# Kernel tuning notes

Hardware: AMD Instinct MI355X
Metric: run time of the kernel (lower is better)

The kernel has to match this reference:

```python
import jax, jax.numpy as jnp
import numpy as np

B, T, N, F_IN = 8, 16, 1000, 16
E = 16000
H, D = 4, 32          # heads, gat_hidden_shape
HL = 64               # lstm hidden
OUT = 8
NEG_SLOPE = 0.2       # PyG GATConv default


def setup_inputs() -> dict:
    key = jax.random.key(0)
    ks = jax.random.split(key, 10)
    def init(k, shape, fan):
        return (jax.random.normal(k, shape, jnp.float32) / np.sqrt(fan)).astype(jnp.float32)
    x = jax.random.normal(ks[0], (B, T, N, F_IN), jnp.float32)
    edge_index = jax.random.randint(ks[1], (2, E), 0, N)
    W_gat = init(ks[2], (F_IN, H * D), F_IN)       # GATConv lin weight
    att_src = init(ks[3], (H, D), D)
    att_dst = init(ks[4], (H, D), D)
    b_gat = jnp.zeros((H * D,), jnp.float32)
    W_ih = init(ks[5], (4 * HL, H * D), H * D)     # LSTM, gate order i,f,g,o
    W_hh = init(ks[6], (4 * HL, HL), HL)
    b_ih = jnp.zeros((4 * HL,), jnp.float32)
    b_hh = jnp.zeros((4 * HL,), jnp.float32)
    W_clf = init(ks[7], (OUT, HL), HL)
    b_clf = jnp.zeros((OUT,), jnp.float32)
    return {"x": x, "edge_index": edge_index, "W_gat": W_gat, "att_src": att_src,
            "att_dst": att_dst, "b_gat": b_gat, "W_ih": W_ih, "W_hh": W_hh,
            "b_ih": b_ih, "b_hh": b_hh, "W_clf": W_clf, "b_clf": b_clf}


def reference(x, edge_index, W_gat, att_src, att_dst, b_gat,
              W_ih, W_hh, b_ih, b_hh, W_clf, b_clf):
    Bx, Tx, Nx, Fx = x.shape
    x_flat = x.reshape(Bx * Tx, Nx, Fx)
    # PyG GATConv adds self-loops by default
    loop = jnp.arange(Nx)
    src = jnp.concatenate([edge_index[0], loop])
    dst = jnp.concatenate([edge_index[1], loop])

    def gat_graph(xg):  # xg: [N, F]
        xp = (xg @ W_gat).reshape(Nx, H, D)                 # [N,H,D]
        a_s = jnp.einsum('nhd,hd->nh', xp, att_src)         # [N,H]
        a_d = jnp.einsum('nhd,hd->nh', xp, att_dst)
        e = jax.nn.leaky_relu(a_s[src] + a_d[dst], NEG_SLOPE)  # [E+N,H]
        m = jax.ops.segment_max(e, dst, num_segments=Nx)       # per-target softmax
        ex = jnp.exp(e - m[dst])
        denom = jax.ops.segment_sum(ex, dst, num_segments=Nx)
        alpha = ex / denom[dst]                                # [E+N,H]
        out = jax.ops.segment_sum(alpha[..., None] * xp[src], dst, num_segments=Nx)
        return out.reshape(Nx, H * D) + b_gat                  # [N, H*D]

    gat = jax.vmap(gat_graph)(x_flat)          # [B*T, N, H*D]
    gat = jax.nn.relu(gat)
    pooled = gat.max(axis=1)                   # global_max_pool -> [B*T, H*D]
    seq = pooled.reshape(Bx, Tx, H * D)

    h0 = jnp.zeros((Bx, HL), jnp.float32)
    c0 = jnp.zeros((Bx, HL), jnp.float32)

    def step(carry, xt):  # xt: [B, H*D]
        h, c = carry
        gates = xt @ W_ih.T + h @ W_hh.T + b_ih + b_hh
        i, f, g, o = jnp.split(gates, 4, axis=-1)
        i, f, o = jax.nn.sigmoid(i), jax.nn.sigmoid(f), jax.nn.sigmoid(o)
        g = jnp.tanh(g)
        c = f * c + i * g
        h = o * jnp.tanh(c)
        return (h, c), None

    (hT, _), _ = jax.lax.scan(step, (h0, c0), seq.transpose(1, 0, 2))
    return hT @ W_clf.T + b_clf                # [B, OUT]
```

## Files before the change

### kernel.cpp

```cpp
#include <hip/hip_runtime.h>
#include <hip/hip_bf16.h>
#include <stdint.h>

namespace {
constexpr int kB = 8, kT = 16, kN = 1000, kF = 16;
constexpr int kE = 16000;
constexpr int kH = 4, kHD = 128;
constexpr int kHL = 64, kOUT = 8;
constexpr int kG = kB * kT;
constexpr float kNeg = 0.2f;
constexpr int kNB = 25;
constexpr int kNPB = 40;
constexpr int kPre = 1024;
constexpr int kNPW = 32;
constexpr int kBCAP = 64;

constexpr size_t CX_WG   = 0;
constexpr size_t CX_ATS  = CX_WG   + 2048;
constexpr size_t CX_ATD  = CX_ATS  + 128;
constexpr size_t CX_BG   = CX_ATD  + 128;
constexpr size_t CX_WIH  = CX_BG   + 128;
constexpr size_t CX_WHH  = CX_WIH  + 32768;
constexpr size_t CX_BIH  = CX_WHH  + 16384;
constexpr size_t CX_BHH  = CX_BIH  + 256;
constexpr size_t CX_WCLF = CX_BHH  + 256;
constexpr size_t CX_BCLF = CX_WCLF + 512;
constexpr size_t CX_TOTAL = CX_BCLF + 8;

constexpr size_t OFF_FLAG  = 0;
constexpr size_t OFF_ROW   = 256;
constexpr size_t OFF_COL   = 4352;
constexpr size_t OFF_POOL  = 68608;
constexpr size_t OFF_CANON = 134400;
constexpr size_t OFF_AS    = 239872;
constexpr size_t OFF_PPART = OFF_AS + (size_t)kG * 288000;
constexpr size_t PPART_BYTES = (size_t)kG * kNB * kHD * 4;
constexpr size_t OFF_BUCKET = OFF_PPART + PPART_BYTES;
constexpr size_t BUCKET_BYTES = (size_t)kN * kBCAP * 4;

constexpr int kSetupBlocks = 41;
}

typedef float v2f __attribute__((ext_vector_type(2)));

__device__ __forceinline__ float bf2f(unsigned short u) {
    return __uint_as_float(((uint32_t)u) << 16);
}
__device__ __forceinline__ float blo(uint32_t u) { return __uint_as_float(u << 16); }
__device__ __forceinline__ float bhi(uint32_t u) { return __uint_as_float(u & 0xffff0000u); }
__device__ __forceinline__ unsigned short f2bf(float f) {
    uint32_t u = __float_as_uint(f);
    uint32_t r = (u + 0x7fff + ((u >> 16) & 1)) >> 16;
    return (unsigned short)r;
}
__device__ __forceinline__ float sigm(float x) { return 1.f / (1.f + __expf(-x)); }

__device__ __forceinline__ int detect_isf(const unsigned short* xs, int t,
                                          int nthr, int* sh_cnt) {
    if (t == 0) *sh_cnt = 0;
    __syncthreads();
    int loc = 0;
    for (int i = t; i < 512; i += nthr) {
        unsigned short u = xs[i];
        int ex = (u >> 7) & 0xff;
        if (u == 0 || (ex >= 97 && ex <= 143)) loc++;
    }
    atomicAdd(sh_cnt, loc);
    __syncthreads();
    return (*sh_cnt >= 410) ? 0 : 1;
}

struct ConvArgs {
    const unsigned short* src[10];
    int n[10];
};

__global__ __launch_bounds__(256) void mega_setup(
        const void* __restrict__ xraw, const int* __restrict__ ei,
        ConvArgs ca,
        const unsigned short* __restrict__ WgR,
        const unsigned short* __restrict__ atsR,
        const unsigned short* __restrict__ atdR,
        int* __restrict__ flag, int* __restrict__ rowdeg, int* __restrict__ col,
        int* __restrict__ bucket, int use_bucket,
        unsigned short* __restrict__ canon,
        unsigned short* __restrict__ xp_all,
        float* __restrict__ as_all, float* __restrict__ ad_all,
        unsigned int* __restrict__ pooled) {
    const int t = threadIdx.x;
    const unsigned short* xs = (const unsigned short*)xraw;

    if (blockIdx.x < 8) {
        __shared__ int dcnt;
        const int isf = detect_isf(xs, t, 256, &dcnt);
        if (blockIdx.x == 0 && t == 0) *flag = isf;
        const int gid = (int)blockIdx.x * 256 + t;
        size_t base = 0;
        for (int s = 0; s < 10; ++s) {
            const int n = ca.n[s];
            if (isf) {
                const float* fp = (const float*)ca.src[s];
                for (int i = gid; i < n; i += 2048) canon[base + i] = f2bf(fp[i]);
            } else {
                const unsigned short* sp = ca.src[s];
                for (int i = gid; i < n; i += 2048) canon[base + i] = sp[i];
            }
            base += (size_t)n;
        }
    } else if (blockIdx.x == 8) {
        for (int i = t; i < kG * kHD; i += 256) pooled[i] = 0u;
    } else if (blockIdx.x < kSetupBlocks) {
        if (use_bucket) {
            const int gid = (int)(blockIdx.x - 9) * 256 + t;
            const int* srcp = ei;
            const int* dstp = ei + kE;
            for (int e = gid; e < kE; e += 32 * 256) {
                const int d = dstp[e];
                const int pos = atomicAdd(&rowdeg[d], 1);
                if (pos < kBCAP) bucket[d * kBCAP + pos] = srcp[e];
            }
        } else if (blockIdx.x == 9) {
            __shared__ int cnt[1024];
            __shared__ int wtot[4];
            const int lane = t & 63, w = t >> 6;
            for (int i = t; i < 1024; i += 256) cnt[i] = 0;
            __syncthreads();
            const int* dst = ei + kE;
            for (int e = t; e < kE; e += 256) atomicAdd(&cnt[dst[e]], 1);
            __syncthreads();
            const int n0 = 4 * t;
            int c0 = cnt[n0], c1 = cnt[n0 + 1], c2 = cnt[n0 + 2], c3 = cnt[n0 + 3];
            int s0 = c0, s1 = s0 + c1, s2 = s1 + c2, s3 = s2 + c3;
            int tot = s3;
#pragma unroll
            for (int sft = 1; sft < 64; sft <<= 1) {
                int v = __shfl_up(tot, sft, 64);
                if (lane >= sft) tot += v;
            }
            if (lane == 63) wtot[w] = tot;
            __syncthreads();
            int wexcl = 0;
            for (int j = 0; j < w; ++j) wexcl += wtot[j];
            const int excl = wexcl + tot - s3;
            if (t == 0) rowdeg[0] = 0;
            if (n0 < kN) {
                rowdeg[n0 + 1] = excl + s0;
                rowdeg[n0 + 2] = excl + s1;
                rowdeg[n0 + 3] = excl + s2;
                rowdeg[n0 + 4] = excl + s3;
            }
            __syncthreads();
            cnt[n0] = excl; cnt[n0 + 1] = excl + s0;
            cnt[n0 + 2] = excl + s1; cnt[n0 + 3] = excl + s2;
            __syncthreads();
            for (int e = t; e < kE; e += 256) {
                int d0 = dst[e];
                int pos = atomicAdd(&cnt[d0], 1);
                col[pos] = ei[e];
            }
        }
    } else {
        __shared__ int dcnt;
        const int isf = detect_isf(xs, t, 256, &dcnt);
        const int lane = t & 63;
        const int wv = t >> 6;
        const int wid = (int)(blockIdx.x - kSetupBlocks) * 4 + wv;

        float wA[kF], wB[kF];
        float as0, as1, ad0, ad1;
        if (isf) {
            const float* wf = (const float*)WgR;
#pragma unroll
            for (int f = 0; f < kF; ++f) {
                const float2 wp = ((const float2*)(wf + (size_t)f * kHD))[lane];
                wA[f] = wp.x; wB[f] = wp.y;
            }
            const float2 sv = ((const float2*)atsR)[lane];
            as0 = sv.x; as1 = sv.y;
            const float2 dv2 = ((const float2*)atdR)[lane];
            ad0 = dv2.x; ad1 = dv2.y;
        } else {
            const uint32_t* w32 = (const uint32_t*)WgR;
#pragma unroll
            for (int f = 0; f < kF; ++f) {
                const uint32_t u = w32[f * 64 + lane];
                wA[f] = blo(u); wB[f] = bhi(u);
            }
            const uint32_t us = ((const uint32_t*)atsR)[lane];
            as0 = blo(us); as1 = bhi(us);
            const uint32_t ud = ((const uint32_t*)atdR)[lane];
            ad0 = blo(ud); ad1 = bhi(ud);
        }

        uint32_t* xp32 = (uint32_t*)xp_all;
        const int nEnd = min(wid * kNPW + kNPW, kG * kN);
        for (int node = wid * kNPW; node < nEnd; ++node) {
            float xv[kF];
            if (isf) {
                const float4* xr4 = (const float4*)((const float*)xraw + (size_t)node * kF);
                const float4 x0 = xr4[0], x1 = xr4[1], x2 = xr4[2], x3 = xr4[3];
                xv[0] = x0.x; xv[1] = x0.y; xv[2]  = x0.z; xv[3]  = x0.w;
                xv[4] = x1.x; xv[5] = x1.y; xv[6]  = x1.z; xv[7]  = x1.w;
                xv[8] = x2.x; xv[9] = x2.y; xv[10] = x2.z; xv[11] = x2.w;
                xv[12] = x3.x; xv[13] = x3.y; xv[14] = x3.z; xv[15] = x3.w;
            } else {
                const uint4* xr4 = (const uint4*)(xs + (size_t)node * kF);
                const uint4 q0 = xr4[0], q1 = xr4[1];
                xv[0]  = blo(q0.x); xv[1]  = bhi(q0.x);
                xv[2]  = blo(q0.y); xv[3]  = bhi(q0.y);
                xv[4]  = blo(q0.z); xv[5]  = bhi(q0.z);
                xv[6]  = blo(q0.w); xv[7]  = bhi(q0.w);
                xv[8]  = blo(q1.x); xv[9]  = bhi(q1.x);
                xv[10] = blo(q1.y); xv[11] = bhi(q1.y);
                xv[12] = blo(q1.z); xv[13] = bhi(q1.z);
                xv[14] = blo(q1.w); xv[15] = bhi(q1.w);
            }
            float vA = 0.f, vB = 0.f;
#pragma unroll
            for (int f = 0; f < kF; ++f) {
                vA = fmaf(xv[f], wA[f], vA);
                vB = fmaf(xv[f], wB[f], vB);
            }
            xp32[(size_t)node * 64 + lane] =
                (uint32_t)f2bf(vA) | ((uint32_t)f2bf(vB) << 16);
            float aS = vA * as0 + vB * as1;
            float aD = vA * ad0 + vB * ad1;
#pragma unroll
            for (int sft = 1; sft < 16; sft <<= 1) {
                aS += __shfl_xor(aS, sft, 64);
                aD += __shfl_xor(aD, sft, 64);
            }
            if ((lane & 15) == 0) {
                as_all[(size_t)node * kH + (lane >> 4)] = aS;
                ad_all[(size_t)node * kH + (lane >> 4)] = aD;
            }
        }
    }
}

__global__ __launch_bounds__(256) void gat_aggregate(
        const int* __restrict__ rowdeg, const int* __restrict__ col,
        const int* __restrict__ bucket, int use_bucket,
        const unsigned short* __restrict__ xp,
        const float* __restrict__ a_s, const float* __restrict__ a_d,
        const unsigned short* __restrict__ bg,
        unsigned int* __restrict__ pooled,
        float* __restrict__ part, int use_part) {
    __shared__ float2 colal[4][4][68];
    __shared__ float pm[4][kHD];

    const int w = threadIdx.x >> 6;
    const int lane = threadIdx.x & 63;
    const int sub = lane >> 4;
    const int cl = lane & 15;
    const int hh = cl >> 2;
    const int xcd = blockIdx.x & 7;
    const int j = blockIdx.x >> 3;
    const int gl = xcd + 8 * (j / kNB);
    const int blk = j % kNB;
    const size_t gn = (size_t)gl * kN;
    const char* xpcl = (const char*)(xp + gn * kHD) + cl * 16;
    const float4* as4 = (const float4*)a_s + gn;
    const float4* ad4 = (const float4*)a_d + gn;
    const uint32_t* bg32 = (const uint32_t*)bg;
    float bgv[8];
#pragma unroll
    for (int jb = 0; jb < 4; ++jb) {
        uint32_t u = bg32[cl * 4 + jb];
        bgv[2 * jb] = blo(u);
        bgv[2 * jb + 1] = bhi(u);
    }
    float pool[8];
#pragma unroll
    for (int jb = 0; jb < 8; ++jb) pool[jb] = 0.f;

    for (int it = 0; it < 10; ++it) {
        const int n = blk * kNPB + it * 4 + w;
        int r0, deg;
        if (use_bucket) {
            r0 = n * kBCAP;
            deg = min(rowdeg[n], kBCAP);
        } else {
            r0 = rowdeg[n];
            deg = rowdeg[n + 1] - r0;
        }
        const int* colb = use_bucket ? bucket : col;
        const int E = deg + 1;
        const float4 dv = ad4[n];
        v2f acc2[4];
#pragma unroll
        for (int jb = 0; jb < 4; ++jb) acc2[jb] = (v2f){0.f, 0.f};
        float dh = 0.f;

        for (int base = 0; base < E; base += 64) {
            const int cnt = min(64, E - base);
            const int cntP = (cnt + 3) & ~3;
            if (lane < cntP) {
                const int eg = base + lane;
                const bool act = lane < cnt;
                const int s = (act && eg < deg) ? colb[r0 + eg] : n;
                float p0 = 0.f, p1 = 0.f, p2 = 0.f, p3 = 0.f;
                if (act) {
                    const float4 av = as4[s];
                    float t0 = av.x + dv.x, t1 = av.y + dv.y;
                    float t2 = av.z + dv.z, t3 = av.w + dv.w;
                    t0 = t0 > 0.f ? t0 : kNeg * t0;
                    t1 = t1 > 0.f ? t1 : kNeg * t1;
                    t2 = t2 > 0.f ? t2 : kNeg * t2;
                    t3 = t3 > 0.f ? t3 : kNeg * t3;
                    p0 = __expf(t0); p1 = __expf(t1);
                    p2 = __expf(t2); p3 = __expf(t3);
                }
                const float cf = __int_as_float(s << 8);
                colal[w][0][lane] = make_float2(cf, p0);
                colal[w][1][lane] = make_float2(cf, p1);
                colal[w][2][lane] = make_float2(cf, p2);
                colal[w][3][lane] = make_float2(cf, p3);
            }
            int e0 = 0;
            for (; e0 + 8 <= cntP; e0 += 8) {
                const float2 cA = colal[w][hh][e0 + sub];
                const float2 cB = colal[w][hh][e0 + 4 + sub];
                const uint4 uA = *(const uint4*)(xpcl + __float_as_int(cA.x));
                const uint4 uB = *(const uint4*)(xpcl + __float_as_int(cB.x));
                const float aA = cA.y, aB = cB.y;
                const v2f aA2 = {aA, aA}, aB2 = {aB, aB};
                acc2[0] += aA2 * (v2f){blo(uA.x), bhi(uA.x)};
                acc2[1] += aA2 * (v2f){blo(uA.y), bhi(uA.y)};
                acc2[2] += aA2 * (v2f){blo(uA.z), bhi(uA.z)};
                acc2[3] += aA2 * (v2f){blo(uA.w), bhi(uA.w)};
                acc2[0] += aB2 * (v2f){blo(uB.x), bhi(uB.x)};
                acc2[1] += aB2 * (v2f){blo(uB.y), bhi(uB.y)};
                acc2[2] += aB2 * (v2f){blo(uB.z), bhi(uB.z)};
                acc2[3] += aB2 * (v2f){blo(uB.w), bhi(uB.w)};
                dh += aA + aB;
            }
            if (e0 < cntP) {
                const float2 cA = colal[w][hh][e0 + sub];
                const uint4 uA = *(const uint4*)(xpcl + __float_as_int(cA.x));
                const float aA = cA.y;
                const v2f aA2 = {aA, aA};
                acc2[0] += aA2 * (v2f){blo(uA.x), bhi(uA.x)};
                acc2[1] += aA2 * (v2f){blo(uA.y), bhi(uA.y)};
                acc2[2] += aA2 * (v2f){blo(uA.z), bhi(uA.z)};
                acc2[3] += aA2 * (v2f){blo(uA.w), bhi(uA.w)};
                dh += aA;
            }
        }
        float acc[8];
#pragma unroll
        for (int jb = 0; jb < 4; ++jb) {
            acc[2 * jb] = acc2[jb].x;
            acc[2 * jb + 1] = acc2[jb].y;
        }
#pragma unroll
        for (int jb = 0; jb < 8; ++jb) {
            acc[jb] += __shfl_xor(acc[jb], 16, 64);
            acc[jb] += __shfl_xor(acc[jb], 32, 64);
        }
        dh += __shfl_xor(dh, 16, 64);
        dh += __shfl_xor(dh, 32, 64);
        const float inv = 1.f / dh;
#pragma unroll
        for (int jb = 0; jb < 8; ++jb) {
            const float o = acc[jb] * inv + bgv[jb];
            pool[jb] = fmaxf(pool[jb], o > 0.f ? o : 0.f);
        }
    }
    if (sub == 0) {
#pragma unroll
        for (int jb = 0; jb < 8; ++jb) pm[w][cl * 8 + jb] = pool[jb];
    }
    __syncthreads();
    if (w == 0 && sub == 0) {
        if (use_part) {
            float* dst = part + ((size_t)gl * kNB + blk) * kHD;
#pragma unroll
            for (int jb = 0; jb < 8; ++jb) {
                const int c = cl * 8 + jb;
                dst[c] = fmaxf(fmaxf(pm[0][c], pm[1][c]), fmaxf(pm[2][c], pm[3][c]));
            }
        } else {
            const size_t gp = (size_t)gl * kHD;
#pragma unroll
            for (int jb = 0; jb < 8; ++jb) {
                const int c = cl * 8 + jb;
                float vmax = fmaxf(fmaxf(pm[0][c], pm[1][c]), fmaxf(pm[2][c], pm[3][c]));
                atomicMax(pooled + gp + c, __float_as_uint(vmax));
            }
        }
    }
}

__global__ __launch_bounds__(256) void lstm_head(
        const float* __restrict__ pooled, const float* __restrict__ part,
        int use_part,
        const unsigned short* __restrict__ Wih,
        const unsigned short* __restrict__ Whh,
        const unsigned short* __restrict__ bih,
        const unsigned short* __restrict__ bhh,
        const unsigned short* __restrict__ Wclf,
        const unsigned short* __restrict__ bclf,
        const int* __restrict__ flag,
        void* __restrict__ out) {
    const int b = blockIdx.x;
    const int r = threadIdx.x;
    __shared__ float xt[kHD];
    __shared__ float hs[kHL];
    __shared__ float gates[4 * kHL];

    uint32_t wih[64];
    const uint32_t* pw = (const uint32_t*)(Wih + (size_t)r * kHD);
#pragma unroll
    for (int j = 0; j < 64; ++j) wih[j] = pw[j];
    uint32_t whh[32];
    const uint32_t* ph = (const uint32_t*)(Whh + (size_t)r * kHL);
#pragma unroll
    for (int j = 0; j < 32; ++j) whh[j] = ph[j];
    const float bias = bf2f(bih[r]) + bf2f(bhh[r]);

    float c_st = 0.f;
    if (r < kHL) hs[r] = 0.f;
    __syncthreads();

    for (int t = 0; t < kT; ++t) {
        const size_t g = (size_t)b * kT + t;
        if (r < kHD) {
            if (use_part) {
                const float* ps = part + g * kNB * kHD + r;
                float v = ps[0];
#pragma unroll
                for (int k = 1; k < kNB; ++k) v = fmaxf(v, ps[(size_t)k * kHD]);
                xt[r] = v;
            } else {
                xt[r] = pooled[g * kHD + r];
            }
        }
        __syncthreads();
        float a0 = 0.f, a1 = 0.f, a2 = 0.f, a3 = 0.f;
#pragma unroll
        for (int j = 0; j < 64; j += 4) {
            uint32_t u0 = wih[j], u1 = wih[j + 1], u2 = wih[j + 2], u3 = wih[j + 3];
            a0 += blo(u0) * xt[2 * j + 0] + bhi(u0) * xt[2 * j + 1];
            a1 += blo(u1) * xt[2 * j + 2] + bhi(u1) * xt[2 * j + 3];
            a2 += blo(u2) * xt[2 * j + 4] + bhi(u2) * xt[2 * j + 5];
            a3 += blo(u3) * xt[2 * j + 6] + bhi(u3) * xt[2 * j + 7];
        }
#pragma unroll
        for (int j = 0; j < 32; j += 4) {
            uint32_t u0 = whh[j], u1 = whh[j + 1], u2 = whh[j + 2], u3 = whh[j + 3];
            a0 += blo(u0) * hs[2 * j + 0] + bhi(u0) * hs[2 * j + 1];
            a1 += blo(u1) * hs[2 * j + 2] + bhi(u1) * hs[2 * j + 3];
            a2 += blo(u2) * hs[2 * j + 4] + bhi(u2) * hs[2 * j + 5];
            a3 += blo(u3) * hs[2 * j + 6] + bhi(u3) * hs[2 * j + 7];
        }
        gates[r] = bias + (a0 + a1) + (a2 + a3);
        __syncthreads();
        if (r < kHL) {
            const float iv = sigm(gates[r]);
            const float fv = sigm(gates[kHL + r]);
            const float gv = tanhf(gates[2 * kHL + r]);
            const float ov = sigm(gates[3 * kHL + r]);
            c_st = fv * c_st + iv * gv;
            hs[r] = ov * tanhf(c_st);
        }
        __syncthreads();
    }
    if (r < kOUT) {
        float acc = bf2f(bclf[r]);
#pragma unroll
        for (int k = 0; k < kHL; ++k) acc += hs[k] * bf2f(Wclf[r * kHL + k]);
        if (*flag) ((float*)out)[b * kOUT + r] = acc;
        else ((__hip_bfloat16*)out)[b * kOUT + r] = __float2bfloat16(acc);
    }
}

extern "C" void kernel_launch(void* const* d_in, const int* in_sizes, int n_in,
                              void* d_out, int out_size, void* d_ws, size_t ws_size,
                              hipStream_t stream) {
    const int* ei = (const int*)d_in[1];

    char* ws = (char*)d_ws;
    int*            flag   = (int*)(ws + OFF_FLAG);
    int*            rowdeg = (int*)(ws + OFF_ROW);
    int*            colv   = (int*)(ws + OFF_COL);
    unsigned int*   pooled = (unsigned int*)(ws + OFF_POOL);
    unsigned short* canon  = (unsigned short*)(ws + OFF_CANON);

    unsigned short* cBg   = canon + CX_BG;
    unsigned short* cWih  = canon + CX_WIH;
    unsigned short* cWhh  = canon + CX_WHH;
    unsigned short* cBih  = canon + CX_BIH;
    unsigned short* cBhh  = canon + CX_BHH;
    unsigned short* cWclf = canon + CX_WCLF;
    unsigned short* cBclf = canon + CX_BCLF;

    float*          a_s = (float*)(ws + OFF_AS);
    float*          a_d = (float*)(ws + OFF_AS + (size_t)kG * 16000);
    unsigned short* xp  = (unsigned short*)(ws + OFF_AS + (size_t)kG * 32000);

    const int use_part   = (ws_size >= OFF_PPART + PPART_BYTES) ? 1 : 0;
    const int use_bucket = (ws_size >= OFF_BUCKET + BUCKET_BYTES) ? 1 : 0;
    float* part   = (float*)(ws + OFF_PPART);
    int*   bucket = (int*)(ws + OFF_BUCKET);

    ConvArgs ca;
    const int sizes[10] = {2048, 128, 128, 128, 32768, 16384, 256, 256, 512, 8};
    const int which[10] = {2, 3, 4, 5, 6, 7, 8, 9, 10, 11};
    for (int i = 0; i < 10; ++i) {
        ca.src[i] = (const unsigned short*)d_in[which[i]];
        ca.n[i] = sizes[i];
    }

    hipMemsetAsync(ws + OFF_ROW, 0, 4096, stream);

    mega_setup<<<kSetupBlocks + kPre, 256, 0, stream>>>(
        d_in[0], ei, ca,
        (const unsigned short*)d_in[2], (const unsigned short*)d_in[3],
        (const unsigned short*)d_in[4],
        flag, rowdeg, colv, bucket, use_bucket, canon, xp, a_s, a_d, pooled);
    gat_aggregate<<<kG * kNB, 256, 0, stream>>>(rowdeg, colv, bucket, use_bucket,
                                                xp, a_s, a_d, cBg,
                                                pooled, part, use_part);
    lstm_head<<<kB, 256, 0, stream>>>((const float*)pooled, part, use_part,
                                      cWih, cWhh, cBih, cBhh,
                                      cWclf, cBclf, flag, d_out);
}
```

Baseline: 200.6 us.

## Add LDS-staged GAT aggregation kernel with one block per graph and head pair

Adds a new gat_lds kernel for the bucketed-adjacency path. Each 1024-thread block loads one graph's projected features for two heads (about 128KB) into LDS, then 16 waves aggregate neighbors from LDS while software-pipelining the bucket and attention-score loads for upcoming nodes. It pools inside the block and writes the pooled results directly, so no partial-pool buffer is needed. The intent is to replace scattered global gathers of neighbor features with LDS reads, at the cost of a large LDS footprint, one block per CU, and a 63-edge-per-node cap in this path.

After: 213.9 us. +6.6%, slower.

```diff
diff --git a/kernel.cpp b/kernel.cpp
--- a/kernel.cpp
+++ b/kernel.cpp
@@ -238,9 +238,127 @@
     }
 }
 
+__global__ __launch_bounds__(1024) void gat_lds(
+        const int* __restrict__ rowdeg, const int* __restrict__ bucket,
+        const unsigned short* __restrict__ xp,
+        const float* __restrict__ a_s, const float* __restrict__ a_d,
+        const unsigned short* __restrict__ bg,
+        float* __restrict__ pooled) {
+    __shared__ uint32_t xp_l[kN * 32];
+    __shared__ int   col_s[16][2][36];
+    __shared__ float p_s[16][2][2][36];
+    __shared__ float2 pm2[16][32];
+
+    const int tid = threadIdx.x;
+    const int wv = tid >> 6, lane = tid & 63;
+    const int gl = blockIdx.x & 127;
+    const int h2 = blockIdx.x >> 7;
+    const int par = lane >> 5;
+    const int c32 = lane & 31;
+    const int hh = c32 >> 4;
+
+    const uint32_t* xpg = (const uint32_t*)(xp + (size_t)gl * kN * kHD) + h2 * 32;
+    for (int idx = tid; idx < kN * 32; idx += 1024) {
+        xp_l[idx] = xpg[(size_t)(idx >> 5) * 64 + (idx & 31)];
+    }
+    if (tid < 128) {
+        const int w0 = tid >> 3, sd = (tid >> 2) & 1, rr = 32 + (tid & 3);
+        col_s[w0][sd][rr] = 0;
+        p_s[w0][0][sd][rr] = 0.f;
+        p_s[w0][1][sd][rr] = 0.f;
+    }
+    __syncthreads();
+
+    const float* asg = a_s + (size_t)gl * kN * kH + h2 * 2;
+    const float* adg = a_d + (size_t)gl * kN * kH + h2 * 2;
+    const uint32_t bgu = ((const uint32_t*)bg)[h2 * 32 + c32];
+    const v2f bgv = {blo(bgu), bhi(bgu)};
+
+    const int cnt = (wv < 8) ? 63 : 62;
+
+    int nA = wv;
+    int degA = min(rowdeg[nA], 63);
+    int sA = (lane < degA) ? bucket[nA * 64 + lane] : nA;
+    float2 avA = *(const float2*)(asg + (size_t)sA * 4);
+    float2 dvA = *(const float2*)(adg + (size_t)nA * 4);
+    int nB = min(nA + 16, kN - 1);
+    int degB = min(rowdeg[nB], 63);
+    int sB = (lane < degB) ? bucket[nB * 64 + lane] : nB;
+    float2 avB = *(const float2*)(asg + (size_t)sB * 4);
+    float2 dvB = *(const float2*)(adg + (size_t)nB * 4);
+
+    v2f pool = {0.f, 0.f};
+    for (int i = 0; i < cnt; ++i) {
+        const int n = nA;
+        const int E = degA + 1;
+        float t0 = avA.x + dvA.x; t0 = t0 > 0.f ? t0 : kNeg * t0;
+        float t1 = avA.y + dvA.y; t1 = t1 > 0.f ? t1 : kNeg * t1;
+        const float p0 = (lane < E) ? __expf(t0) : 0.f;
+        const float p1 = (lane < E) ? __expf(t1) : 0.f;
+        col_s[wv][lane & 1][lane >> 1] = sA * 32;
+        p_s[wv][0][lane & 1][lane >> 1] = p0;
+        p_s[wv][1][lane & 1][lane >> 1] = p1;
+
+        const int nC = min(n + 32, kN - 1);
+        const int degC = min(rowdeg[nC], 63);
+        const int sC0 = bucket[nC * 64 + lane];
+
+        const int rounds = (E + 1) >> 1;
+        const int ng = (rounds + 3) >> 2;
+        const int* cb = &col_s[wv][par][0];
+        const float* pb = &p_s[wv][hh][par][0];
+        v2f acc = {0.f, 0.f};
+        float dh = 0.f;
+        int4 off4 = *(const int4*)cb;
+        float4 al4 = *(const float4*)pb;
+        for (int g = 1; g <= ng; ++g) {
+            const int4 off4n = *(const int4*)(cb + 4 * g);
+            const float4 al4n = *(const float4*)(pb + 4 * g);
+            const uint32_t u0 = xp_l[off4.x + c32];
+            const uint32_t u1 = xp_l[off4.y + c32];
+            const uint32_t u2 = xp_l[off4.z + c32];
+            const uint32_t u3 = xp_l[off4.w + c32];
+            acc += (v2f){al4.x, al4.x} * (v2f){blo(u0), bhi(u0)};
+            acc += (v2f){al4.y, al4.y} * (v2f){blo(u1), bhi(u1)};
+            acc += (v2f){al4.z, al4.z} * (v2f){blo(u2), bhi(u2)};
+            acc += (v2f){al4.w, al4.w} * (v2f){blo(u3), bhi(u3)};
+            dh += (al4.x + al4.y) + (al4.z + al4.w);
+            off4 = off4n; al4 = al4n;
+        }
+
+        const int sC = (lane < degC) ? sC0 : nC;
+        const float2 avC = *(const float2*)(asg + (size_t)sC * 4);
+        const float2 dvC = *(const float2*)(adg + (size_t)nC * 4);
+
+        acc.x += __shfl_xor(acc.x, 32, 64);
+        acc.y += __shfl_xor(acc.y, 32, 64);
+        dh += __shfl_xor(dh, 32, 64);
+        const float inv = 1.f / dh;
+        const float ox = acc.x * inv + bgv.x;
+        const float oy = acc.y * inv + bgv.y;
+        pool.x = fmaxf(pool.x, ox);
+        pool.y = fmaxf(pool.y, oy);
+
+        nA = nB; degA = degB; sA = sB; avA = avB; dvA = dvB;
+        nB = nC; degB = degC; sB = sC; avB = avC; dvB = dvC;
+    }
+
+    if (par == 0) pm2[wv][c32] = make_float2(pool.x, pool.y);
+    __syncthreads();
+    if (tid < 32) {
+        float2 m = pm2[0][tid];
+#pragma unroll
+        for (int jw = 1; jw < 16; ++jw) {
+            const float2 v = pm2[jw][tid];
+            m.x = fmaxf(m.x, v.x);
+            m.y = fmaxf(m.y, v.y);
+        }
+        *(float2*)(pooled + (size_t)gl * kHD + h2 * 64 + 2 * tid) = m;
+    }
+}
+
 __global__ __launch_bounds__(256) void gat_aggregate(
         const int* __restrict__ rowdeg, const int* __restrict__ col,
-        const int* __restrict__ bucket, int use_bucket,
         const unsigned short* __restrict__ xp,
         const float* __restrict__ a_s, const float* __restrict__ a_d,
         const unsigned short* __restrict__ bg,
@@ -274,17 +392,39 @@
 #pragma unroll
     for (int jb = 0; jb < 8; ++jb) pool[jb] = 0.f;
 
+    auto pairBody = [&](v2f* acc2, float& dh, int e0) {
+        const float2 cA = colal[w][hh][e0 + sub];
+        const float2 cB = colal[w][hh][e0 + 4 + sub];
+        const uint4 uA = *(const uint4*)(xpcl + __float_as_int(cA.x));
+        const uint4 uB = *(const uint4*)(xpcl + __float_as_int(cB.x));
+        const float aA = cA.y, aB = cB.y;
+        const v2f aA2 = {aA, aA}, aB2 = {aB, aB};
+        acc2[0] += aA2 * (v2f){blo(uA.x), bhi(uA.x)};
+        acc2[1] += aA2 * (v2f){blo(uA.y), bhi(uA.y)};
+        acc2[2] += aA2 * (v2f){blo(uA.z), bhi(uA.z)};
+        acc2[3] += aA2 * (v2f){blo(uA.w), bhi(uA.w)};
+        acc2[0] += aB2 * (v2f){blo(uB.x), bhi(uB.x)};
+        acc2[1] += aB2 * (v2f){blo(uB.y), bhi(uB.y)};
+        acc2[2] += aB2 * (v2f){blo(uB.z), bhi(uB.z)};
+        acc2[3] += aB2 * (v2f){blo(uB.w), bhi(uB.w)};
+        dh += aA + aB;
+    };
+    auto singleBody = [&](v2f* acc2, float& dh, int e0) {
+        const float2 cA = colal[w][hh][e0 + sub];
+        const uint4 uA = *(const uint4*)(xpcl + __float_as_int(cA.x));
+        const float aA = cA.y;
+        const v2f aA2 = {aA, aA};
+        acc2[0] += aA2 * (v2f){blo(uA.x), bhi(uA.x)};
+        acc2[1] += aA2 * (v2f){blo(uA.y), bhi(uA.y)};
+        acc2[2] += aA2 * (v2f){blo(uA.z), bhi(uA.z)};
+        acc2[3] += aA2 * (v2f){blo(uA.w), bhi(uA.w)};
+        dh += aA;
+    };
+
     for (int it = 0; it < 10; ++it) {
         const int n = blk * kNPB + it * 4 + w;
-        int r0, deg;
-        if (use_bucket) {
-            r0 = n * kBCAP;
-            deg = min(rowdeg[n], kBCAP);
-        } else {
-            r0 = rowdeg[n];
-            deg = rowdeg[n + 1] - r0;
-        }
-        const int* colb = use_bucket ? bucket : col;
+        const int r0 = rowdeg[n];
+        const int deg = rowdeg[n + 1] - r0;
         const int E = deg + 1;
         const float4 dv = ad4[n];
         v2f acc2[4];
@@ -298,7 +438,7 @@
             if (lane < cntP) {
                 const int eg = base + lane;
                 const bool act = lane < cnt;
-                const int s = (act && eg < deg) ? colb[r0 + eg] : n;
+                const int s = (act && eg < deg) ? col[r0 + eg] : n;
                 float p0 = 0.f, p1 = 0.f, p2 = 0.f, p3 = 0.f;
                 if (act) {
                     const float4 av = as4[s];
@@ -318,34 +458,8 @@
                 colal[w][3][lane] = make_float2(cf, p3);
             }
             int e0 = 0;
-            for (; e0 + 8 <= cntP; e0 += 8) {
-                const float2 cA = colal[w][hh][e0 + sub];
-                const float2 cB = colal[w][hh][e0 + 4 + sub];
-                const uint4 uA = *(const uint4*)(xpcl + __float_as_int(cA.x));
-                const uint4 uB = *(const uint4*)(xpcl + __float_as_int(cB.x));
-                const float aA = cA.y, aB = cB.y;
-                const v2f aA2 = {aA, aA}, aB2 = {aB, aB};
-                acc2[0] += aA2 * (v2f){blo(uA.x), bhi(uA.x)};
-                acc2[1] += aA2 * (v2f){blo(uA.y), bhi(uA.y)};
-                acc2[2] += aA2 * (v2f){blo(uA.z), bhi(uA.z)};
-                acc2[3] += aA2 * (v2f){blo(uA.w), bhi(uA.w)};
-                acc2[0] += aB2 * (v2f){blo(uB.x), bhi(uB.x)};
-                acc2[1] += aB2 * (v2f){blo(uB.y), bhi(uB.y)};
-                acc2[2] += aB2 * (v2f){blo(uB.z), bhi(uB.z)};
-                acc2[3] += aB2 * (v2f){blo(uB.w), bhi(uB.w)};
-                dh += aA + aB;
-            }
-            if (e0 < cntP) {
-                const float2 cA = colal[w][hh][e0 + sub];
-                const uint4 uA = *(const uint4*)(xpcl + __float_as_int(cA.x));
-                const float aA = cA.y;
-                const v2f aA2 = {aA, aA};
-                acc2[0] += aA2 * (v2f){blo(uA.x), bhi(uA.x)};
-                acc2[1] += aA2 * (v2f){blo(uA.y), bhi(uA.y)};
-                acc2[2] += aA2 * (v2f){blo(uA.z), bhi(uA.z)};
-                acc2[3] += aA2 * (v2f){blo(uA.w), bhi(uA.w)};
-                dh += aA;
-            }
+            for (; e0 + 8 <= cntP; e0 += 8) pairBody(acc2, dh, e0);
+            if (e0 < cntP) singleBody(acc2, dh, e0);
         }
         float acc[8];
 #pragma unroll
@@ -519,10 +633,17 @@
         (const unsigned short*)d_in[2], (const unsigned short*)d_in[3],
         (const unsigned short*)d_in[4],
         flag, rowdeg, colv, bucket, use_bucket, canon, xp, a_s, a_d, pooled);
-    gat_aggregate<<<kG * kNB, 256, 0, stream>>>(rowdeg, colv, bucket, use_bucket,
-                                                xp, a_s, a_d, cBg,
-                                                pooled, part, use_part);
-    lstm_head<<<kB, 256, 0, stream>>>((const float*)pooled, part, use_part,
-                                      cWih, cWhh, cBih, cBhh,
-                                      cWclf, cBclf, flag, d_out);
-}
+    if (use_bucket) {
+        gat_lds<<<256, 1024, 0, stream>>>(rowdeg, bucket, xp, a_s, a_d, cBg,
+                                          (float*)pooled);
+        lstm_head<<<kB, 256, 0, stream>>>((const float*)pooled, part, 0,
+                                          cWih, cWhh, cBih, cBhh,
+                                          cWclf, cBclf, flag, d_out);
+    } else {
+        gat_aggregate<<<kG * kNB, 256, 0, stream>>>(rowdeg, colv, xp, a_s, a_d,
+                                                    cBg, pooled, part, use_part);
+        lstm_head<<<kB, 256, 0, stream>>>((const float*)pooled, part, use_part,
+                                          cWih, cWhh, cBih, cBhh,
+                                          cWclf, cBclf, flag, d_out);
+    }
+}
```
